# Optimization experiments

Hardware: AMD Instinct MI355X
Metric: run time of the kernel (lower is better)

The kernel has to match this reference:

```python
import jax, jax.numpy as jnp
import numpy as np

N_HEADS = 16

def setup_inputs() -> dict:
    key = jax.random.key(0)
    k1, k2, k3 = jax.random.split(key, 3)
    B, T, C = 2, 2048, 1024
    x = jax.random.normal(k1, (B, T, C), dtype=jnp.float32)
    # torch Linear(n_embed, 3*n_embed, bias=False) -> store as [in, out]
    W_qkv = jax.random.normal(k2, (C, 3 * C), dtype=jnp.float32) * (1.0 / np.sqrt(C))
    W_proj = jax.random.normal(k3, (C, C), dtype=jnp.float32) * (1.0 / np.sqrt(C))
    return {"x": x, "W_qkv": W_qkv, "W_proj": W_proj}

def reference(x, W_qkv, W_proj):
    B, T, C = x.shape
    H = N_HEADS
    d = C // H
    qkv = x @ W_qkv                                   # [B, T, 3C]
    q, k, v = jnp.split(qkv, 3, axis=-1)
    # [B, T, C] -> [B, H, T, d]
    q = q.reshape(B, T, H, d).transpose(0, 2, 1, 3)
    k = k.reshape(B, T, H, d).transpose(0, 2, 1, 3)
    v = v.reshape(B, T, H, d).transpose(0, 2, 1, 3)
    scale = 1.0 / np.sqrt(d).astype(np.float32)
    wei = jnp.einsum('bhqd,bhkd->bhqk', q, k) * scale  # [B, H, T, T]
    causal = jnp.tril(jnp.ones((T, T), dtype=bool))
    wei = jnp.where(causal[None, None, :, :], wei, jnp.float32(-jnp.inf))
    wei = jax.nn.softmax(wei, axis=-1)
    out = jnp.einsum('bhqk,bhkd->bhqd', wei, v)        # [B, H, T, d]
    out = out.transpose(0, 2, 1, 3).reshape(B, T, C)
    return out @ W_proj
```

## Files before the change

### kernel.cpp

```cpp
#include <hip/hip_runtime.h>
#include <stdint.h>

typedef __attribute__((ext_vector_type(8))) short short8v;
typedef __attribute__((ext_vector_type(4))) float float4v;
typedef __attribute__((ext_vector_type(4))) unsigned short ushort4v;
typedef __attribute__((ext_vector_type(2))) unsigned int uint2v;
typedef __attribute__((ext_vector_type(4))) unsigned int uint4v;

#define B_SZ 2
#define T_SEQ 2048
#define C_EMB 1024
#define NH 16
#define DH 64
#define M_ROWS (B_SZ * T_SEQ)
#define CEXP 0.18033688f
#define DEFER_THR 44.3614f

__device__ __forceinline__ unsigned short f2bf(float f) {
    unsigned int u = __float_as_uint(f);
    u += 0x7FFFu + ((u >> 16) & 1u);
    return (unsigned short)(u >> 16);
}

__device__ __forceinline__ unsigned int cvtpk_bf16(float lo, float hi) {
    unsigned int r;
    asm("v_cvt_pk_bf16_f32 %0, %1, %2" : "=v"(r) : "v"(lo), "v"(hi));
    return r;
}

__device__ __forceinline__ void gload_lds16(const void* g, void* s) {
    __builtin_amdgcn_global_load_lds(
        (const __attribute__((address_space(1))) void*)g,
        (__attribute__((address_space(3))) void*)s, 16, 0, 0);
}

__device__ __forceinline__ void memfence_sched() { asm volatile("" ::: "memory"); }

__device__ __forceinline__ void block_barrier() {
    memfence_sched();
    __builtin_amdgcn_s_barrier();
    memfence_sched();
}

__global__ __launch_bounds__(256) void k_cvt_x(const float* __restrict__ in,
                                               unsigned short* __restrict__ out, int n4) {
    int i = blockIdx.x * 256 + threadIdx.x;
    if (i >= n4) return;
    float4v v = ((const float4v*)in)[i];
    ushort4v o;
    o.x = f2bf(v.x); o.y = f2bf(v.y); o.z = f2bf(v.z); o.w = f2bf(v.w);
    ((ushort4v*)out)[i] = o;
}

__global__ __launch_bounds__(256) void k_transpose_cvt(const float* __restrict__ in,
                                                       unsigned short* __restrict__ out,
                                                       int R, int C) {
    __shared__ float tile[64][65];
    int c0 = blockIdx.x * 64;
    int r0 = blockIdx.y * 64;
#pragma unroll
    for (int i = 0; i < 16; ++i) {
        int e = i * 256 + threadIdx.x;
        int r = e >> 6, c = e & 63;
        tile[r][c] = in[(size_t)(r0 + r) * C + c0 + c];
    }
    __syncthreads();
#pragma unroll
    for (int i = 0; i < 16; ++i) {
        int e = i * 256 + threadIdx.x;
        int r = e >> 6, c = e & 63;
        out[(size_t)(c0 + r) * R + r0 + c] = f2bf(tile[c][r]);
    }
}

__global__ __launch_bounds__(256) void k_gemm_bt(const unsigned short* __restrict__ A,
                                                 const unsigned short* __restrict__ Bt,
                                                 void* __restrict__ Cout,
                                                 int M, int N, int K, int out_f32) {
    __shared__ __align__(16) unsigned short As[3][128 * 32];
    __shared__ __align__(16) unsigned short Bs[3][128 * 32];

    const int tid = threadIdx.x;
    const int lane = tid & 63;
    const int w = tid >> 6;
    const int lr = lane & 15;
    const int lg = lane >> 4;
    const int wr = (w >> 1) * 64;
    const int wc = (w & 1) * 64;

    const int gx = gridDim.x;
    const int nwg = gx * gridDim.y;
    const int lin = blockIdx.y * gx + blockIdx.x;
    const int q8 = nwg >> 3;
    const int wg = (lin & 7) * q8 + (lin >> 3);
    const int mb = wg / gx;
    const int nb = wg - mb * gx;
    const int m0 = mb * 128;
    const int n0 = nb * 128;

    const unsigned short* aptr = A + (size_t)(m0 + (tid >> 2)) * K + (tid & 3) * 8;
    const unsigned short* bptr = Bt + (size_t)(n0 + (tid >> 2)) * K + (tid & 3) * 8;

    float4v acc[4][4];
#pragma unroll
    for (int i = 0; i < 4; ++i)
#pragma unroll
        for (int j = 0; j < 4; ++j) acc[i][j] = (float4v){0.f, 0.f, 0.f, 0.f};

#define G_STAGE(buf, t)                                                        \
    do {                                                                       \
        const int k0_ = (t) * 32;                                              \
        gload_lds16(aptr + k0_, &As[buf][tid * 8]);                            \
        gload_lds16(aptr + (size_t)64 * K + k0_, &As[buf][2048 + tid * 8]);    \
        gload_lds16(bptr + k0_, &Bs[buf][tid * 8]);                            \
        gload_lds16(bptr + (size_t)64 * K + k0_, &Bs[buf][2048 + tid * 8]);    \
    } while (0)

    const int NT = K >> 5;
    G_STAGE(0, 0);
    G_STAGE(1, 1);

    int cur = 0;
    for (int t = 0; t < NT; ++t) {
        if (t < NT - 1) { asm volatile("s_waitcnt vmcnt(4)" ::: "memory"); }
        else           { asm volatile("s_waitcnt vmcnt(0)" ::: "memory"); }
        block_barrier();
        if (t + 2 < NT) { G_STAGE((cur == 0 ? 2 : cur - 1), t + 2); }

        short8v af[4], bf[4];
#pragma unroll
        for (int i = 0; i < 4; ++i)
            af[i] = *(const short8v*)&As[cur][(wr + i * 16 + lr) * 32 + lg * 8];
#pragma unroll
        for (int i = 0; i < 4; ++i)
            bf[i] = *(const short8v*)&Bs[cur][(wc + i * 16 + lr) * 32 + lg * 8];
        __builtin_amdgcn_s_setprio(1);
#pragma unroll
        for (int mi = 0; mi < 4; ++mi)
#pragma unroll
            for (int ni = 0; ni < 4; ++ni)
                acc[mi][ni] = __builtin_amdgcn_mfma_f32_16x16x32_bf16(af[mi], bf[ni],
                                                                      acc[mi][ni], 0, 0, 0);
        __builtin_amdgcn_s_setprio(0);
        cur = (cur == 2) ? 0 : cur + 1;
    }
#undef G_STAGE

#pragma unroll
    for (int mi = 0; mi < 4; ++mi) {
#pragma unroll
        for (int ni = 0; ni < 4; ++ni) {
            int row = m0 + wr + mi * 16 + lg * 4;
            int col = n0 + wc + ni * 16 + lr;
            if (out_f32) {
                float* Cf = (float*)Cout;
#pragma unroll
                for (int r = 0; r < 4; ++r) Cf[(size_t)(row + r) * N + col] = acc[mi][ni][r];
            } else {
                unsigned short* Cb = (unsigned short*)Cout;
#pragma unroll
                for (int r = 0; r < 4; ++r) Cb[(size_t)(row + r) * N + col] = f2bf(acc[mi][ni][r]);
            }
        }
    }
}

__global__ __launch_bounds__(256) void k_transpose_v(const unsigned short* __restrict__ qkv,
                                                     unsigned short* __restrict__ vt) {
    __shared__ unsigned short tile[64][72];
    int t0 = blockIdx.x * 64;
    int bh = blockIdx.y;
    int b = bh >> 4, h = bh & 15;
#pragma unroll
    for (int i = 0; i < 2; ++i) {
        int e = i * 256 + threadIdx.x;
        int tt = e >> 3, db = (e & 7) * 8;
        short8v v = *(const short8v*)&qkv[(size_t)(b * T_SEQ + t0 + tt) * (3 * C_EMB)
                                          + 2 * C_EMB + h * DH + db];
#pragma unroll
        for (int j = 0; j < 8; ++j) tile[tt][db + j] = (unsigned short)v[j];
    }
    __syncthreads();
#pragma unroll
    for (int i = 0; i < 2; ++i) {
        int e = i * 256 + threadIdx.x;
        int d = e >> 3, tb = (e & 7) * 8;
        short8v ov;
#pragma unroll
        for (int j = 0; j < 8; ++j)
            ov[j] = (short)tile[(tb & 32) + ((tb >> 3) & 3) * 4 + 16 * (j >> 2) + (j & 3)][d];
        *(short8v*)&vt[(size_t)(bh * DH + d) * T_SEQ + t0 + tb] = ov;
    }
}

template<bool MASK>
__device__ __forceinline__ void attn_tile(const unsigned short* __restrict__ Ksb,
                                          const unsigned short* __restrict__ Vsb,
                                          short8v qa0, short8v qa1,
                                          float4v (&o)[4], float& m_run, float& l_run,
                                          int lr, int lg, int wq) {
    const int swz = lr & 7;
    float4v s[4];
    __builtin_amdgcn_s_setprio(1);
#pragma unroll
    for (int sub = 0; sub < 4; ++sub) {
        const unsigned short* rowp = Ksb + (sub * 16 + lr) * 64;
        short8v kb0 = *(const short8v*)&rowp[(lg ^ swz) * 8];
        short8v kb1 = *(const short8v*)&rowp[((4 + lg) ^ swz) * 8];
        float4v acc = (float4v){0.f, 0.f, 0.f, 0.f};
        acc = __builtin_amdgcn_mfma_f32_16x16x32_bf16(kb0, qa0, acc, 0, 0, 0);
        acc = __builtin_amdgcn_mfma_f32_16x16x32_bf16(kb1, qa1, acc, 0, 0, 0);
        s[sub] = acc;
    }
    __builtin_amdgcn_s_setprio(0);
    if (MASK) {
#pragma unroll
        for (int sub = 0; sub < 4; ++sub)
#pragma unroll
            for (int r = 0; r < 4; ++r)
                s[sub][r] = (sub * 16 + lg * 4 + r <= wq + lr) ? s[sub][r] : -1e30f;
    }
    float pmax = s[0][0];
#pragma unroll
    for (int sub = 0; sub < 4; ++sub)
#pragma unroll
        for (int r = 0; r < 4; ++r) pmax = fmaxf(pmax, s[sub][r]);

    if (__any(pmax - m_run > DEFER_THR)) {
        float fm = fmaxf(pmax, __shfl_xor(pmax, 16));
        fm = fmaxf(fm, __shfl_xor(fm, 32));
        float nm = fmaxf(m_run, fm);
        float alpha = exp2f((m_run - nm) * CEXP);
        m_run = nm;
#pragma unroll
        for (int n = 0; n < 4; ++n) o[n] *= alpha;
        l_run *= alpha;
    }
    const float mc = m_run * CEXP;
    float p[4][4];
    float rowsum = 0.f;
#pragma unroll
    for (int sub = 0; sub < 4; ++sub)
#pragma unroll
        for (int r = 0; r < 4; ++r) {
            p[sub][r] = exp2f(__builtin_fmaf(s[sub][r], CEXP, -mc));
            rowsum += p[sub][r];
        }
    l_run += rowsum;

#pragma unroll
    for (int kk = 0; kk < 2; ++kk) {
        uint4v up;
        up.x = cvtpk_bf16(p[2 * kk][0],     p[2 * kk][1]);
        up.y = cvtpk_bf16(p[2 * kk][2],     p[2 * kk][3]);
        up.z = cvtpk_bf16(p[2 * kk + 1][0], p[2 * kk + 1][1]);
        up.w = cvtpk_bf16(p[2 * kk + 1][2], p[2 * kk + 1][3]);
        short8v pb = *(short8v*)&up;
        __builtin_amdgcn_s_setprio(1);
#pragma unroll
        for (int n = 0; n < 4; ++n) {
            short8v vb = *(const short8v*)&Vsb[(n * 16 + lr) * 64 + ((kk * 4 + lg) ^ swz) * 8];
            o[n] = __builtin_amdgcn_mfma_f32_16x16x32_bf16(vb, pb, o[n], 0, 0, 0);
        }
        __builtin_amdgcn_s_setprio(0);
    }
}

__global__ __launch_bounds__(256, 4) void k_attn(const unsigned short* __restrict__ qkv,
                                                 const unsigned short* __restrict__ vt,
                                                 unsigned short* __restrict__ aout) {
    __shared__ __align__(16) unsigned short Ks[2][64 * 64];
    __shared__ __align__(16) unsigned short Vs[2][64 * 64];

    const int tid = threadIdx.x;
    const int lane = tid & 63;
    const int w = tid >> 6;
    const int lr = lane & 15;
    const int lg = lane >> 4;

    const int bh = blockIdx.x;
    const int q0 = ((int)gridDim.y - 1 - (int)blockIdx.y) * 64;
    const int b = bh >> 4, h = bh & 15;

    const unsigned short* qrowp =
        qkv + (size_t)(b * T_SEQ + q0 + w * 16 + lr) * (3 * C_EMB) + h * DH + lg * 8;
    short8v qa0 = *(const short8v*)qrowp;
    short8v qa1 = *(const short8v*)(qrowp + 32);

    float4v o[4];
    float m_run = -1e30f, l_run = 0.f;
#pragma unroll
    for (int n = 0; n < 4; ++n) o[n] = (float4v){0.f, 0.f, 0.f, 0.f};

    const int lc = ((tid & 7) ^ ((tid >> 3) & 7)) * 8;
    const unsigned short* kbase =
        qkv + (size_t)(b * T_SEQ + (tid >> 3)) * (3 * C_EMB) + C_EMB + h * DH + lc;
    const unsigned short* vbase = vt + (size_t)(bh * DH + (tid >> 3)) * T_SEQ + lc;

    const int wq = w * 16;
    const int nt = q0 / 64 + 1;

    gload_lds16(kbase, &Ks[0][tid * 8]);
    gload_lds16(kbase + (size_t)32 * 3 * C_EMB, &Ks[0][2048 + tid * 8]);
    gload_lds16(vbase, &Vs[0][tid * 8]);
    gload_lds16(vbase + (size_t)32 * T_SEQ, &Vs[0][2048 + tid * 8]);

    int cur = 0;
    for (int t = 0; t < nt - 1; ++t) {
        const size_t kv0 = (size_t)(t + 1) * 64;
        gload_lds16(kbase + kv0 * 3 * C_EMB, &Ks[cur ^ 1][tid * 8]);
        gload_lds16(kbase + (kv0 + 32) * 3 * C_EMB, &Ks[cur ^ 1][2048 + tid * 8]);
        gload_lds16(vbase + kv0, &Vs[cur ^ 1][tid * 8]);
        gload_lds16(vbase + (size_t)32 * T_SEQ + kv0, &Vs[cur ^ 1][2048 + tid * 8]);
        asm volatile("s_waitcnt vmcnt(4)" ::: "memory");
        block_barrier();
        attn_tile<false>(&Ks[cur][0], &Vs[cur][0], qa0, qa1, o, m_run, l_run, lr, lg, wq);
        block_barrier();
        cur ^= 1;
    }
    asm volatile("s_waitcnt vmcnt(0)" ::: "memory");
    block_barrier();
    attn_tile<true>(&Ks[cur][0], &Vs[cur][0], qa0, qa1, o, m_run, l_run, lr, lg, wq);

    float lt = l_run;
    lt += __shfl_xor(lt, 16);
    lt += __shfl_xor(lt, 32);
    const float rl = 1.0f / lt;
    const int trow = b * T_SEQ + q0 + wq + lr;
#pragma unroll
    for (int n = 0; n < 4; ++n) {
        uint2v uu;
        uu.x = cvtpk_bf16(o[n][0] * rl, o[n][1] * rl);
        uu.y = cvtpk_bf16(o[n][2] * rl, o[n][3] * rl);
        *(uint2v*)&aout[(size_t)trow * C_EMB + h * DH + n * 16 + lg * 4] = uu;
    }
}

extern "C" void kernel_launch(void* const* d_in, const int* in_sizes, int n_in,
                              void* d_out, int out_size, void* d_ws, size_t ws_size,
                              hipStream_t stream) {
    const float* x = (const float*)d_in[0];
    const float* Wqkv = (const float*)d_in[1];
    const float* Wproj = (const float*)d_in[2];
    float* out = (float*)d_out;

    unsigned short* xb     = (unsigned short*)d_ws;
    unsigned short* wqkvT  = xb + (size_t)M_ROWS * C_EMB;
    unsigned short* wprojT = wqkvT + (size_t)3 * C_EMB * C_EMB;
    unsigned short* qkvb   = wprojT + (size_t)C_EMB * C_EMB;
    unsigned short* vtb    = qkvb + (size_t)M_ROWS * 3 * C_EMB;
    unsigned short* attb   = vtb + (size_t)M_ROWS * C_EMB;

    k_cvt_x<<<(M_ROWS * C_EMB / 4 + 255) / 256, 256, 0, stream>>>(x, xb, M_ROWS * C_EMB / 4);
    k_transpose_cvt<<<dim3(3 * C_EMB / 64, C_EMB / 64), 256, 0, stream>>>(Wqkv, wqkvT, C_EMB, 3 * C_EMB);
    k_transpose_cvt<<<dim3(C_EMB / 64, C_EMB / 64), 256, 0, stream>>>(Wproj, wprojT, C_EMB, C_EMB);
    k_gemm_bt<<<dim3(3 * C_EMB / 128, M_ROWS / 128), 256, 0, stream>>>(xb, wqkvT, (void*)qkvb,
                                                                       M_ROWS, 3 * C_EMB, C_EMB, 0);
    k_transpose_v<<<dim3(T_SEQ / 64, B_SZ * NH), 256, 0, stream>>>(qkvb, vtb);
    k_attn<<<dim3(B_SZ * NH, T_SEQ / 64), 256, 0, stream>>>(qkvb, vtb, attb);
    k_gemm_bt<<<dim3(C_EMB / 128, M_ROWS / 128), 256, 0, stream>>>(attb, wprojT, (void*)out,
                                                                   M_ROWS, C_EMB, C_EMB, 1);
}
```

Measured before the change: 117.0 us.

## Process two 64-row query groups per attention block to reuse K/V tiles

Each attention block now handles 128 query rows as two 64-row groups that share every staged K/V tile, which halves global K/V loads and LDS staging per query row. Causal handling gets three tile modes: full for both groups, masked diagonal for the first group, and second-group-only for the last tile. The grid halves to 512 blocks, and register pressure roughly doubles for the accumulators and softmax state, which may reduce occupancy under the 4-wave launch bound.

New measurement: 129.5 us. 10.7% more time.

```diff
diff --git a/kernel.cpp b/kernel.cpp
--- a/kernel.cpp
+++ b/kernel.cpp
@@ -193,74 +193,97 @@
     }
 }
 
-template<bool MASK>
-__device__ __forceinline__ void attn_tile(const unsigned short* __restrict__ Ksb,
-                                          const unsigned short* __restrict__ Vsb,
-                                          short8v qa0, short8v qa1,
-                                          float4v (&o)[4], float& m_run, float& l_run,
-                                          int lr, int lg, int wq) {
+template<int MODE>
+__device__ __forceinline__ void attn_tile2(const unsigned short* __restrict__ Ksb,
+                                           const unsigned short* __restrict__ Vsb,
+                                           const short8v (&qa)[2][2],
+                                           float4v (&o)[2][4], float (&m_run)[2], float (&l_run)[2],
+                                           int lr, int lg, int wq) {
     const int swz = lr & 7;
-    float4v s[4];
+    float4v s[2][4];
     __builtin_amdgcn_s_setprio(1);
 #pragma unroll
     for (int sub = 0; sub < 4; ++sub) {
         const unsigned short* rowp = Ksb + (sub * 16 + lr) * 64;
         short8v kb0 = *(const short8v*)&rowp[(lg ^ swz) * 8];
         short8v kb1 = *(const short8v*)&rowp[((4 + lg) ^ swz) * 8];
-        float4v acc = (float4v){0.f, 0.f, 0.f, 0.f};
-        acc = __builtin_amdgcn_mfma_f32_16x16x32_bf16(kb0, qa0, acc, 0, 0, 0);
-        acc = __builtin_amdgcn_mfma_f32_16x16x32_bf16(kb1, qa1, acc, 0, 0, 0);
-        s[sub] = acc;
+        if (MODE != 2) {
+            float4v a0 = (float4v){0.f, 0.f, 0.f, 0.f};
+            a0 = __builtin_amdgcn_mfma_f32_16x16x32_bf16(kb0, qa[0][0], a0, 0, 0, 0);
+            a0 = __builtin_amdgcn_mfma_f32_16x16x32_bf16(kb1, qa[0][1], a0, 0, 0, 0);
+            s[0][sub] = a0;
+        }
+        float4v a1 = (float4v){0.f, 0.f, 0.f, 0.f};
+        a1 = __builtin_amdgcn_mfma_f32_16x16x32_bf16(kb0, qa[1][0], a1, 0, 0, 0);
+        a1 = __builtin_amdgcn_mfma_f32_16x16x32_bf16(kb1, qa[1][1], a1, 0, 0, 0);
+        s[1][sub] = a1;
     }
     __builtin_amdgcn_s_setprio(0);
-    if (MASK) {
+    if (MODE == 1) {
 #pragma unroll
         for (int sub = 0; sub < 4; ++sub)
 #pragma unroll
             for (int r = 0; r < 4; ++r)
-                s[sub][r] = (sub * 16 + lg * 4 + r <= wq + lr) ? s[sub][r] : -1e30f;
-    }
-    float pmax = s[0][0];
-#pragma unroll
-    for (int sub = 0; sub < 4; ++sub)
-#pragma unroll
-        for (int r = 0; r < 4; ++r) pmax = fmaxf(pmax, s[sub][r]);
-
-    if (__any(pmax - m_run > DEFER_THR)) {
-        float fm = fmaxf(pmax, __shfl_xor(pmax, 16));
-        fm = fmaxf(fm, __shfl_xor(fm, 32));
-        float nm = fmaxf(m_run, fm);
-        float alpha = exp2f((m_run - nm) * CEXP);
-        m_run = nm;
-#pragma unroll
-        for (int n = 0; n < 4; ++n) o[n] *= alpha;
-        l_run *= alpha;
-    }
-    const float mc = m_run * CEXP;
-    float p[4][4];
-    float rowsum = 0.f;
-#pragma unroll
-    for (int sub = 0; sub < 4; ++sub)
-#pragma unroll
-        for (int r = 0; r < 4; ++r) {
-            p[sub][r] = exp2f(__builtin_fmaf(s[sub][r], CEXP, -mc));
-            rowsum += p[sub][r];
-        }
-    l_run += rowsum;
+                s[0][sub][r] = (sub * 16 + lg * 4 + r <= wq + lr) ? s[0][sub][r] : -1e30f;
+    }
+    if (MODE == 2) {
+#pragma unroll
+        for (int sub = 0; sub < 4; ++sub)
+#pragma unroll
+            for (int r = 0; r < 4; ++r)
+                s[1][sub][r] = (sub * 16 + lg * 4 + r <= wq + lr) ? s[1][sub][r] : -1e30f;
+    }
+
+    uint4v pbu[2][2];
+#pragma unroll
+    for (int g = 0; g < 2; ++g) {
+        if (MODE == 2 && g == 0) continue;
+        float pmax = s[g][0][0];
+#pragma unroll
+        for (int sub = 0; sub < 4; ++sub)
+#pragma unroll
+            for (int r = 0; r < 4; ++r) pmax = fmaxf(pmax, s[g][sub][r]);
+
+        if (__any(pmax - m_run[g] > DEFER_THR)) {
+            float fm = fmaxf(pmax, __shfl_xor(pmax, 16));
+            fm = fmaxf(fm, __shfl_xor(fm, 32));
+            float nm = fmaxf(m_run[g], fm);
+            float alpha = exp2f((m_run[g] - nm) * CEXP);
+            m_run[g] = nm;
+#pragma unroll
+            for (int n = 0; n < 4; ++n) o[g][n] *= alpha;
+            l_run[g] *= alpha;
+        }
+        const float mc = m_run[g] * CEXP;
+        float rowsum = 0.f;
+#pragma unroll
+        for (int kk = 0; kk < 2; ++kk) {
+            float p0[4], p1[4];
+#pragma unroll
+            for (int r = 0; r < 4; ++r) {
+                p0[r] = exp2f(__builtin_fmaf(s[g][2 * kk][r], CEXP, -mc));
+                p1[r] = exp2f(__builtin_fmaf(s[g][2 * kk + 1][r], CEXP, -mc));
+                rowsum += p0[r] + p1[r];
+            }
+            pbu[g][kk].x = cvtpk_bf16(p0[0], p0[1]);
+            pbu[g][kk].y = cvtpk_bf16(p0[2], p0[3]);
+            pbu[g][kk].z = cvtpk_bf16(p1[0], p1[1]);
+            pbu[g][kk].w = cvtpk_bf16(p1[2], p1[3]);
+        }
+        l_run[g] += rowsum;
+    }
 
 #pragma unroll
     for (int kk = 0; kk < 2; ++kk) {
-        uint4v up;
-        up.x = cvtpk_bf16(p[2 * kk][0],     p[2 * kk][1]);
-        up.y = cvtpk_bf16(p[2 * kk][2],     p[2 * kk][3]);
-        up.z = cvtpk_bf16(p[2 * kk + 1][0], p[2 * kk + 1][1]);
-        up.w = cvtpk_bf16(p[2 * kk + 1][2], p[2 * kk + 1][3]);
-        short8v pb = *(short8v*)&up;
+        short8v pb0 = *(short8v*)&pbu[0][kk];
+        short8v pb1 = *(short8v*)&pbu[1][kk];
         __builtin_amdgcn_s_setprio(1);
 #pragma unroll
         for (int n = 0; n < 4; ++n) {
             short8v vb = *(const short8v*)&Vsb[(n * 16 + lr) * 64 + ((kk * 4 + lg) ^ swz) * 8];
-            o[n] = __builtin_amdgcn_mfma_f32_16x16x32_bf16(vb, pb, o[n], 0, 0, 0);
+            if (MODE != 2)
+                o[0][n] = __builtin_amdgcn_mfma_f32_16x16x32_bf16(vb, pb0, o[0][n], 0, 0, 0);
+            o[1][n] = __builtin_amdgcn_mfma_f32_16x16x32_bf16(vb, pb1, o[1][n], 0, 0, 0);
         }
         __builtin_amdgcn_s_setprio(0);
     }
@@ -279,18 +302,25 @@
     const int lg = lane >> 4;
 
     const int bh = blockIdx.x;
-    const int q0 = ((int)gridDim.y - 1 - (int)blockIdx.y) * 64;
+    const int q0 = ((int)gridDim.y - 1 - (int)blockIdx.y) * 128;
     const int b = bh >> 4, h = bh & 15;
 
-    const unsigned short* qrowp =
-        qkv + (size_t)(b * T_SEQ + q0 + w * 16 + lr) * (3 * C_EMB) + h * DH + lg * 8;
-    short8v qa0 = *(const short8v*)qrowp;
-    short8v qa1 = *(const short8v*)(qrowp + 32);
-
-    float4v o[4];
-    float m_run = -1e30f, l_run = 0.f;
-#pragma unroll
-    for (int n = 0; n < 4; ++n) o[n] = (float4v){0.f, 0.f, 0.f, 0.f};
+    short8v qa[2][2];
+#pragma unroll
+    for (int g = 0; g < 2; ++g) {
+        const unsigned short* qrowp =
+            qkv + (size_t)(b * T_SEQ + q0 + g * 64 + w * 16 + lr) * (3 * C_EMB) + h * DH + lg * 8;
+        qa[g][0] = *(const short8v*)qrowp;
+        qa[g][1] = *(const short8v*)(qrowp + 32);
+    }
+
+    float4v o[2][4];
+    float m_run[2] = {-1e30f, -1e30f};
+    float l_run[2] = {0.f, 0.f};
+#pragma unroll
+    for (int g = 0; g < 2; ++g)
+#pragma unroll
+        for (int n = 0; n < 4; ++n) o[g][n] = (float4v){0.f, 0.f, 0.f, 0.f};
 
     const int lc = ((tid & 7) ^ ((tid >> 3) & 7)) * 8;
     const unsigned short* kbase =
@@ -298,41 +328,53 @@
     const unsigned short* vbase = vt + (size_t)(bh * DH + (tid >> 3)) * T_SEQ + lc;
 
     const int wq = w * 16;
-    const int nt = q0 / 64 + 1;
-
-    gload_lds16(kbase, &Ks[0][tid * 8]);
-    gload_lds16(kbase + (size_t)32 * 3 * C_EMB, &Ks[0][2048 + tid * 8]);
-    gload_lds16(vbase, &Vs[0][tid * 8]);
-    gload_lds16(vbase + (size_t)32 * T_SEQ, &Vs[0][2048 + tid * 8]);
+    const int nt = q0 / 64 + 2;
+
+#define A_STAGE(buf, t)                                                            \
+    do {                                                                           \
+        const size_t kv0_ = (size_t)(t) * 64;                                      \
+        gload_lds16(kbase + kv0_ * 3 * C_EMB, &Ks[buf][tid * 8]);                  \
+        gload_lds16(kbase + (kv0_ + 32) * 3 * C_EMB, &Ks[buf][2048 + tid * 8]);    \
+        gload_lds16(vbase + kv0_, &Vs[buf][tid * 8]);                              \
+        gload_lds16(vbase + (size_t)32 * T_SEQ + kv0_, &Vs[buf][2048 + tid * 8]);  \
+    } while (0)
+
+    A_STAGE(0, 0);
 
     int cur = 0;
-    for (int t = 0; t < nt - 1; ++t) {
-        const size_t kv0 = (size_t)(t + 1) * 64;
-        gload_lds16(kbase + kv0 * 3 * C_EMB, &Ks[cur ^ 1][tid * 8]);
-        gload_lds16(kbase + (kv0 + 32) * 3 * C_EMB, &Ks[cur ^ 1][2048 + tid * 8]);
-        gload_lds16(vbase + kv0, &Vs[cur ^ 1][tid * 8]);
-        gload_lds16(vbase + (size_t)32 * T_SEQ + kv0, &Vs[cur ^ 1][2048 + tid * 8]);
+    for (int t = 0; t < nt - 2; ++t) {
+        A_STAGE(cur ^ 1, t + 1);
         asm volatile("s_waitcnt vmcnt(4)" ::: "memory");
         block_barrier();
-        attn_tile<false>(&Ks[cur][0], &Vs[cur][0], qa0, qa1, o, m_run, l_run, lr, lg, wq);
+        attn_tile2<0>(&Ks[cur][0], &Vs[cur][0], qa, o, m_run, l_run, lr, lg, wq);
         block_barrier();
         cur ^= 1;
     }
+    A_STAGE(cur ^ 1, nt - 1);
+    asm volatile("s_waitcnt vmcnt(4)" ::: "memory");
+    block_barrier();
+    attn_tile2<1>(&Ks[cur][0], &Vs[cur][0], qa, o, m_run, l_run, lr, lg, wq);
+    block_barrier();
+    cur ^= 1;
     asm volatile("s_waitcnt vmcnt(0)" ::: "memory");
     block_barrier();
-    attn_tile<true>(&Ks[cur][0], &Vs[cur][0], qa0, qa1, o, m_run, l_run, lr, lg, wq);
-
-    float lt = l_run;
-    lt += __shfl_xor(lt, 16);
-    lt += __shfl_xor(lt, 32);
-    const float rl = 1.0f / lt;
-    const int trow = b * T_SEQ + q0 + wq + lr;
-#pragma unroll
-    for (int n = 0; n < 4; ++n) {
-        uint2v uu;
-        uu.x = cvtpk_bf16(o[n][0] * rl, o[n][1] * rl);
-        uu.y = cvtpk_bf16(o[n][2] * rl, o[n][3] * rl);
-        *(uint2v*)&aout[(size_t)trow * C_EMB + h * DH + n * 16 + lg * 4] = uu;
+    attn_tile2<2>(&Ks[cur][0], &Vs[cur][0], qa, o, m_run, l_run, lr, lg, wq);
+#undef A_STAGE
+
+#pragma unroll
+    for (int g = 0; g < 2; ++g) {
+        float lt = l_run[g];
+        lt += __shfl_xor(lt, 16);
+        lt += __shfl_xor(lt, 32);
+        const float rl = 1.0f / lt;
+        const int trow = b * T_SEQ + q0 + g * 64 + wq + lr;
+#pragma unroll
+        for (int n = 0; n < 4; ++n) {
+            uint2v uu;
+            uu.x = cvtpk_bf16(o[g][n][0] * rl, o[g][n][1] * rl);
+            uu.y = cvtpk_bf16(o[g][n][2] * rl, o[g][n][3] * rl);
+            *(uint2v*)&aout[(size_t)trow * C_EMB + h * DH + n * 16 + lg * 4] = uu;
+        }
     }
 }
 
@@ -357,7 +399,7 @@
     k_gemm_bt<<<dim3(3 * C_EMB / 128, M_ROWS / 128), 256, 0, stream>>>(xb, wqkvT, (void*)qkvb,
                                                                        M_ROWS, 3 * C_EMB, C_EMB, 0);
     k_transpose_v<<<dim3(T_SEQ / 64, B_SZ * NH), 256, 0, stream>>>(qkvb, vtb);
-    k_attn<<<dim3(B_SZ * NH, T_SEQ / 64), 256, 0, stream>>>(qkvb, vtb, attb);
+    k_attn<<<dim3(B_SZ * NH, T_SEQ / 128), 256, 0, stream>>>(qkvb, vtb, attb);
     k_gemm_bt<<<dim3(C_EMB / 128, M_ROWS / 128), 256, 0, stream>>>(attb, wprojT, (void*)out,
                                                                    M_ROWS, C_EMB, C_EMB, 1);
 }
```
